# Kernel tuning notes

Hardware: AMD Instinct MI355X
Metric: run time of the kernel (lower is better)

Reference implementation:

```python
import jax, jax.numpy as jnp
import numpy as np

B, N, C, K = 16, 1024, 192, 9
H = 4 * C  # hidden of second MLP pair


def _gelu(x):
    return jax.nn.gelu(x, approximate=False)  # torch nn.GELU default is exact erf


def _mlp(x, w1, b1, w2, b2):
    # TwoLayerNN: Linear -> GELU -> Linear
    return _gelu(x @ w1.T + b1) @ w2.T + b2


def _linear_init(key, out_d, in_d):
    k1, k2 = jax.random.split(key)
    s = 1.0 / np.sqrt(in_d)
    w = jax.random.uniform(k1, (out_d, in_d), minval=-s, maxval=s, dtype=jnp.float32)
    b = jax.random.uniform(k2, (out_d,), minval=-s, maxval=s, dtype=jnp.float32)
    return w, b


def setup_inputs() -> dict:
    key = jax.random.key(0)
    ks = jax.random.split(key, 10)
    x = jax.random.normal(ks[0], (B, N, C), dtype=jnp.float32)
    il1_w1, il1_b1 = _linear_init(ks[1], C, C)
    il1_w2, il1_b2 = _linear_init(ks[2], C, C)
    ol1_w1, ol1_b1 = _linear_init(ks[3], C, C)
    ol1_w2, ol1_b2 = _linear_init(ks[4], C, C)
    il2_w1, il2_b1 = _linear_init(ks[5], H, C)
    il2_w2, il2_b2 = _linear_init(ks[6], C, H)
    ol2_w1, ol2_b1 = _linear_init(ks[7], H, C)
    ol2_w2, ol2_b2 = _linear_init(ks[8], C, H)
    fc_w, fc_b = _linear_init(ks[9], C, 2 * C)  # Conv1d(2C, C, 1) == Linear(2C->C)
    return dict(x=x,
                il1_w1=il1_w1, il1_b1=il1_b1, il1_w2=il1_w2, il1_b2=il1_b2,
                fc_w=fc_w, fc_b=fc_b,
                ol1_w1=ol1_w1, ol1_b1=ol1_b1, ol1_w2=ol1_w2, ol1_b2=ol1_b2,
                il2_w1=il2_w1, il2_b1=il2_b1, il2_w2=il2_w2, il2_b2=il2_b2,
                ol2_w1=ol2_w1, ol2_b1=ol2_b1, ol2_w2=ol2_w2, ol2_b2=ol2_b2)


def reference(x, il1_w1, il1_b1, il1_w2, il1_b2, fc_w, fc_b,
              ol1_w1, ol1_b1, ol1_w2, ol1_b2,
              il2_w1, il2_b1, il2_w2, il2_b2,
              ol2_w1, ol2_b1, ol2_w2, ol2_b2):
    Bx, Nx, Cx = x.shape
    # 1) dense similarity + KNN graph (indices only; no grad path through sim)
    sim = jnp.einsum('bnc,bmc->bnm', x, x)                       # [B,N,N]
    _, graph = jax.lax.top_k(sim, K)                             # [B,N,K] int32
    shortcut = x
    # 2) node transform then gather-max aggregation
    h = _mlp(x.reshape(Bx * Nx, Cx), il1_w1, il1_b1, il1_w2, il1_b2).reshape(Bx, Nx, Cx)
    nb = jnp.take_along_axis(h[:, None, :, :], graph[:, :, :, None], axis=2)  # [B,N,K,C]
    agg = jnp.max(nb - h[:, :, None, :], axis=2)                 # [B,N,C]
    # 3) stack along new last dim then flatten -> interleaved channels [x_c0,agg_c0,x_c1,...]
    cat = jnp.stack([h, agg], axis=-1).reshape(Bx, Nx, 2 * Cx)   # [B,N,2C]
    h = cat @ fc_w.T + fc_b                                      # Conv1d k=1 == Linear
    h = _mlp(_gelu(h).reshape(Bx * Nx, Cx), ol1_w1, ol1_b1, ol1_w2, ol1_b2).reshape(Bx, Nx, Cx)
    x1 = h + shortcut
    # 4) FFN block (two TwoLayerNNs with external GELU between them)
    f = _mlp(x1.reshape(Bx * Nx, Cx), il2_w1, il2_b1, il2_w2, il2_b2)
    f = _mlp(_gelu(f), ol2_w1, ol2_b1, ol2_w2, ol2_b2).reshape(Bx, Nx, Cx)
    return f + x1
```

## Files before the change

kernel.cpp:

```cpp
#include <hip/hip_runtime.h>
#include <hip/hip_bf16.h>
#include <math.h>

#define DEVINL __device__ __forceinline__

typedef __attribute__((ext_vector_type(4))) float f32x4;
typedef __attribute__((ext_vector_type(8))) short s16x8;

DEVINL unsigned short f2bf(float f) {
  union { float f; unsigned u; } v; v.f = f;
  unsigned r = v.u + 0x7FFFu + ((v.u >> 16) & 1u);
  return (unsigned short)(r >> 16);
}
DEVINL float bf2f(unsigned short s) {
  union { unsigned u; float f; } v; v.u = ((unsigned)s) << 16;
  return v.f;
}
DEVINL float gelu_exact(float x) {
  return 0.5f * x * (1.0f + erff(x * 0.70710678118654752f));
}

__global__ __launch_bounds__(256) void conv_kernel(const float* __restrict__ x,
                                                   unsigned short* __restrict__ xh,
                                                   unsigned short* __restrict__ xl) {
  int i = blockIdx.x * 256 + threadIdx.x;
  float4 v = ((const float4*)x)[i];
  float f[4] = {v.x, v.y, v.z, v.w};
  unsigned short h[4], l[4];
#pragma unroll
  for (int j = 0; j < 4; ++j) {
    h[j] = f2bf(f[j]);
    l[j] = f2bf(f[j] - bf2f(h[j]));
  }
  uint2 uh, ul;
  uh.x = (unsigned)h[0] | ((unsigned)h[1] << 16);
  uh.y = (unsigned)h[2] | ((unsigned)h[3] << 16);
  ul.x = (unsigned)l[0] | ((unsigned)l[1] << 16);
  ul.y = (unsigned)l[2] | ((unsigned)l[3] << 16);
  ((uint2*)xh)[i] = uh;
  ((uint2*)xl)[i] = ul;
}

__global__ __launch_bounds__(512)
#if __has_attribute(amdgpu_waves_per_eu)
__attribute__((amdgpu_waves_per_eu(4, 4)))
#endif
void simtopk_kernel(const unsigned short* __restrict__ xh,
                    const unsigned short* __restrict__ xl,
                    int* __restrict__ graph) {
  const int tid  = threadIdx.x;
  const int lane = tid & 63;
  const int w    = tid >> 6;
  const int rb   = blockIdx.x;
  const int b    = blockIdx.y;
  const int wm   = w >> 2, wn = w & 3;

  __shared__ __align__(16) char smem[57472];
  unsigned short* colsH = (unsigned short*)smem;
  unsigned short* colsL = (unsigned short*)(smem + 24576);
  float* simt = (float*)(smem + 49152);
  float* Lv = (float*)smem;
  int*   Li = (int*)(smem + 18432);
  float* Mv = (float*)(smem + 36864);
  int*   Mi = (int*)(smem + 41472);

  const unsigned short* xhb = xh + (size_t)b * (1024 * 192);
  const unsigned short* xlb = xl + (size_t)b * (1024 * 192);

  s16x8 ah[6], al[6];
#pragma unroll
  for (int ks = 0; ks < 6; ++ks) {
    int r = rb * 32 + wm * 16 + (lane & 15);
    size_t off = (size_t)r * 192 + ks * 32 + (lane >> 4) * 8;
    ah[ks] = *(const s16x8*)(xhb + off);
    al[ks] = *(const s16x8*)(xlb + off);
  }

  auto stage = [&](int ct) {
#pragma unroll
    for (int i = 0; i < 3; ++i) {
      int c = tid + i * 512;
      int row = c / 24, cc = c - row * 24;
      size_t goff = (size_t)(ct * 64 + row) * 192 + (size_t)((cc ^ (row & 7)) * 8);
      unsigned short* dstH = colsH + (size_t)c * 8;
      unsigned short* dstL = colsL + (size_t)c * 8;
      __builtin_amdgcn_global_load_lds((const __attribute__((address_space(1))) void*)(xhb + goff),
                                       (__attribute__((address_space(3))) void*)dstH, 16, 0, 0);
      __builtin_amdgcn_global_load_lds((const __attribute__((address_space(1))) void*)(xlb + goff),
                                       (__attribute__((address_space(3))) void*)dstL, 16, 0, 0);
    }
  };

  float tv[9]; int tix[9];
#pragma unroll
  for (int k = 0; k < 9; ++k) { tv[k] = -3.0e38f; tix[k] = 1 << 30; }

  stage(0);
  __syncthreads();

  for (int ct = 0; ct < 16; ++ct) {
    f32x4 a0 = 0, a1 = 0, a2 = 0;

#pragma unroll
    for (int ks = 0; ks < 6; ++ks) {
      const int chk = ks * 4 + (lane >> 4);
      const int rc  = wn * 16 + (lane & 15);
      const int si  = rc * 192 + ((chk ^ (rc & 7)) * 8);
      s16x8 bh = *(const s16x8*)&colsH[si];
      s16x8 bl = *(const s16x8*)&colsL[si];
      a0 = __builtin_amdgcn_mfma_f32_16x16x32_bf16(ah[ks], bh, a0, 0, 0, 0);
      a1 = __builtin_amdgcn_mfma_f32_16x16x32_bf16(ah[ks], bl, a1, 0, 0, 0);
      a2 = __builtin_amdgcn_mfma_f32_16x16x32_bf16(al[ks], bh, a2, 0, 0, 0);
    }

#pragma unroll
    for (int r = 0; r < 4; ++r) {
      int rr = wm * 16 + (lane >> 4) * 4 + r;
      int cc = wn * 16 + (lane & 15);
      simt[rr * 65 + cc] = a0[r] + a1[r] + a2[r];
    }
    __syncthreads();

    if (ct < 15) stage(ct + 1);

    {
      int r = tid >> 4, q = tid & 15;
#pragma unroll
      for (int j = 0; j < 4; ++j) {
        float v = simt[r * 65 + q * 4 + j];
        int   c = ct * 64 + q * 4 + j;
        if (v > tv[8]) {
          tv[8] = v; tix[8] = c;
#pragma unroll
          for (int s = 8; s > 0; --s) {
            if (tv[s] > tv[s - 1]) {
              float fv = tv[s]; tv[s] = tv[s - 1]; tv[s - 1] = fv;
              int   fi = tix[s]; tix[s] = tix[s - 1]; tix[s - 1] = fi;
            }
          }
        }
      }
    }
    __syncthreads();
  }

#pragma unroll
  for (int k = 0; k < 9; ++k) { Lv[tid * 9 + k] = tv[k]; Li[tid * 9 + k] = tix[k]; }
  __syncthreads();

  if (tid < 128) {
    int r = tid >> 2, p = tid & 3;
    float fv[9]; int fi[9];
#pragma unroll
    for (int k = 0; k < 9; ++k) { fv[k] = -3.0e38f; fi[k] = 1 << 30; }
    for (int s4 = 0; s4 < 4; ++s4) {
      int base = (r * 16 + p * 4 + s4) * 9;
#pragma unroll
      for (int k = 0; k < 9; ++k) {
        float v = Lv[base + k]; int c = Li[base + k];
        bool better = (v > fv[8]) || (v == fv[8] && c < fi[8]);
        if (better) {
          fv[8] = v; fi[8] = c;
#pragma unroll
          for (int s = 8; s > 0; --s) {
            bool up = (fv[s] > fv[s - 1]) || (fv[s] == fv[s - 1] && fi[s] < fi[s - 1]);
            if (up) {
              float a = fv[s]; fv[s] = fv[s - 1]; fv[s - 1] = a;
              int  ii = fi[s]; fi[s] = fi[s - 1]; fi[s - 1] = ii;
            }
          }
        }
      }
    }
#pragma unroll
    for (int k = 0; k < 9; ++k) { Mv[tid * 9 + k] = fv[k]; Mi[tid * 9 + k] = fi[k]; }
  }
  __syncthreads();

  if (tid < 32) {
    float fv[9]; int fi[9];
#pragma unroll
    for (int k = 0; k < 9; ++k) { fv[k] = -3.0e38f; fi[k] = 1 << 30; }
    for (int p = 0; p < 4; ++p) {
      int base = (tid * 4 + p) * 9;
#pragma unroll
      for (int k = 0; k < 9; ++k) {
        float v = Mv[base + k]; int c = Mi[base + k];
        bool better = (v > fv[8]) || (v == fv[8] && c < fi[8]);
        if (better) {
          fv[8] = v; fi[8] = c;
#pragma unroll
          for (int s = 8; s > 0; --s) {
            bool up = (fv[s] > fv[s - 1]) || (fv[s] == fv[s - 1] && fi[s] < fi[s - 1]);
            if (up) {
              float a = fv[s]; fv[s] = fv[s - 1]; fv[s - 1] = a;
              int  ii = fi[s]; fi[s] = fi[s - 1]; fi[s - 1] = ii;
            }
          }
        }
      }
    }
    int* gout = graph + ((size_t)b * 1024 + rb * 32 + tid) * 9;
#pragma unroll
    for (int k = 0; k < 9; ++k) gout[k] = fi[k];
  }
}

__global__ __launch_bounds__(256) void agg_kernel(const unsigned short* __restrict__ h,
                                                  const int* __restrict__ graph,
                                                  unsigned short* __restrict__ cat) {
  int gid  = blockIdx.x * 4 + (threadIdx.x >> 6);
  int lane = threadIdx.x & 63;
  int b = gid >> 10;
  int n = gid & 1023;
  const unsigned short* hb = h + (size_t)b * (1024 * 192);
  const int* g = graph + (size_t)gid * 9;
  float hn[3];
#pragma unroll
  for (int j = 0; j < 3; ++j) hn[j] = bf2f(hb[(size_t)n * 192 + lane + j * 64]);
  float ag[3] = {-3.0e38f, -3.0e38f, -3.0e38f};
  for (int k = 0; k < 9; ++k) {
    int idx = g[k];
#pragma unroll
    for (int j = 0; j < 3; ++j) {
      float v = bf2f(hb[(size_t)idx * 192 + lane + j * 64]) - hn[j];
      ag[j] = fmaxf(ag[j], v);
    }
  }
  unsigned* crow = (unsigned*)cat + (size_t)gid * 192;
#pragma unroll
  for (int j = 0; j < 3; ++j) {
    int c = lane + j * 64;
    crow[c] = (unsigned)f2bf(hn[j]) | ((unsigned)f2bf(ag[j]) << 16);
  }
}

template <bool GELU_, bool RESID>
__global__ __launch_bounds__(256) void gemm_kernel(const unsigned short* __restrict__ A,
                                                   const float* __restrict__ W,
                                                   const float* __restrict__ bias,
                                                   const float* __restrict__ resid,
                                                   unsigned short* __restrict__ outb,
                                                   float* __restrict__ outf,
                                                   int N, int K) {
  __shared__ unsigned short As[2][128 * 64];
  __shared__ unsigned short Ws[2][64 * 64];

  const int tid  = threadIdx.x;
  const int lane = tid & 63;
  const int w    = tid >> 6;
  const int m0   = blockIdx.x * 128;
  const int n0   = blockIdx.y * 64;

  auto stageA = [&](int buf, int kt) {
    const unsigned short* gA = A + (size_t)m0 * K + kt * 64;
#pragma unroll
    for (int i = 0; i < 4; ++i) {
      int chunk = w * 4 + i;
      const unsigned short* src = gA + (size_t)(chunk * 8 + (lane >> 3)) * K + (lane & 7) * 8;
      unsigned short* dst = &As[buf][chunk * 512];
      __builtin_amdgcn_global_load_lds((const __attribute__((address_space(1))) void*)src,
                                       (__attribute__((address_space(3))) void*)dst, 16, 0, 0);
    }
  };
  auto stageW = [&](int buf, int kt) {
#pragma unroll
    for (int i = 0; i < 4; ++i) {
      int idx = tid + i * 256;
      int n = idx >> 4, kq = idx & 15;
      float4 v = *(const float4*)(W + (size_t)(n0 + n) * K + kt * 64 + kq * 4);
      uint2 u;
      u.x = (unsigned)f2bf(v.x) | ((unsigned)f2bf(v.y) << 16);
      u.y = (unsigned)f2bf(v.z) | ((unsigned)f2bf(v.w) << 16);
      *(uint2*)&Ws[buf][n * 64 + kq * 4] = u;
    }
  };

  stageA(0, 0);
  stageW(0, 0);
  __syncthreads();

  const int wm = w >> 1, wn = w & 1;
  f32x4 acc[4][2];
#pragma unroll
  for (int a = 0; a < 4; ++a)
#pragma unroll
    for (int c = 0; c < 2; ++c) acc[a][c] = 0;

  const int nk = K >> 6;
  for (int kt = 0; kt < nk; ++kt) {
    const int cur = kt & 1;
    if (kt + 1 < nk) { stageA(cur ^ 1, kt + 1); stageW(cur ^ 1, kt + 1); }
#pragma unroll
    for (int ks = 0; ks < 2; ++ks) {
      const int ko = ks * 32 + (lane >> 4) * 8;
      s16x8 af[4], bfr[2];
#pragma unroll
      for (int m2 = 0; m2 < 4; ++m2)
        af[m2] = *(const s16x8*)&As[cur][(wm * 64 + m2 * 16 + (lane & 15)) * 64 + ko];
#pragma unroll
      for (int n2 = 0; n2 < 2; ++n2)
        bfr[n2] = *(const s16x8*)&Ws[cur][(wn * 32 + n2 * 16 + (lane & 15)) * 64 + ko];
#pragma unroll
      for (int m2 = 0; m2 < 4; ++m2)
#pragma unroll
        for (int n2 = 0; n2 < 2; ++n2)
          acc[m2][n2] = __builtin_amdgcn_mfma_f32_16x16x32_bf16(af[m2], bfr[n2], acc[m2][n2], 0, 0, 0);
    }
    __syncthreads();
  }

#pragma unroll
  for (int m2 = 0; m2 < 4; ++m2)
#pragma unroll
    for (int n2 = 0; n2 < 2; ++n2)
#pragma unroll
      for (int r = 0; r < 4; ++r) {
        int row = m0 + wm * 64 + m2 * 16 + (lane >> 4) * 4 + r;
        int col = n0 + wn * 32 + n2 * 16 + (lane & 15);
        float v = acc[m2][n2][r] + bias[col];
        if (GELU_) v = gelu_exact(v);
        if (RESID) v += resid[(size_t)row * N + col];
        size_t o = (size_t)row * N + col;
        if (outb) outb[o] = f2bf(v);
        if (outf) outf[o] = v;
      }
}

extern "C" void kernel_launch(void* const* d_in, const int* in_sizes, int n_in,
                              void* d_out, int out_size, void* d_ws, size_t ws_size,
                              hipStream_t stream) {
  (void)in_sizes; (void)n_in; (void)out_size; (void)ws_size;
  const float* x      = (const float*)d_in[0];
  const float* il1_w1 = (const float*)d_in[1];
  const float* il1_b1 = (const float*)d_in[2];
  const float* il1_w2 = (const float*)d_in[3];
  const float* il1_b2 = (const float*)d_in[4];
  const float* fc_w   = (const float*)d_in[5];
  const float* fc_b   = (const float*)d_in[6];
  const float* ol1_w1 = (const float*)d_in[7];
  const float* ol1_b1 = (const float*)d_in[8];
  const float* ol1_w2 = (const float*)d_in[9];
  const float* ol1_b2 = (const float*)d_in[10];
  const float* il2_w1 = (const float*)d_in[11];
  const float* il2_b1 = (const float*)d_in[12];
  const float* il2_w2 = (const float*)d_in[13];
  const float* il2_b2 = (const float*)d_in[14];
  const float* ol2_w1 = (const float*)d_in[15];
  const float* ol2_b1 = (const float*)d_in[16];
  const float* ol2_w2 = (const float*)d_in[17];
  const float* ol2_b2 = (const float*)d_in[18];

  char* ws = (char*)d_ws;
  const size_t SZ = 16384ull * 192 * 2;
  unsigned short* xbf  = (unsigned short*)(ws);
  unsigned short* t13  = (unsigned short*)(ws + SZ);
  unsigned short* hbuf = (unsigned short*)(ws + 2 * SZ);
  unsigned short* t2   = (unsigned short*)(ws + 3 * SZ);
  unsigned short* x1b  = (unsigned short*)(ws + 4 * SZ);
  unsigned short* catg = (unsigned short*)(ws + 5 * SZ);
  float*          x1f  = (float*)(ws + 7 * SZ);
  unsigned short* uv   = (unsigned short*)(ws + 9 * SZ);
  unsigned short* xlo  = uv;
  int*            graph = (int*)(ws + 13 * SZ);

  conv_kernel<<<3072, 256, 0, stream>>>(x, xbf, xlo);
  simtopk_kernel<<<dim3(32, 16), 512, 0, stream>>>(xbf, xlo, graph);
  gemm_kernel<true,  false><<<dim3(128, 3), 256, 0, stream>>>(xbf, il1_w1, il1_b1, nullptr, t13, nullptr, 192, 192);
  gemm_kernel<false, false><<<dim3(128, 3), 256, 0, stream>>>(t13, il1_w2, il1_b2, nullptr, hbuf, nullptr, 192, 192);
  agg_kernel<<<4096, 256, 0, stream>>>(hbuf, graph, catg);
  gemm_kernel<true,  false><<<dim3(128, 3), 256, 0, stream>>>(catg, fc_w, fc_b, nullptr, t2, nullptr, 192, 384);
  gemm_kernel<true,  false><<<dim3(128, 3), 256, 0, stream>>>(t2, ol1_w1, ol1_b1, nullptr, t13, nullptr, 192, 192);
  gemm_kernel<false, true ><<<dim3(128, 3), 256, 0, stream>>>(t13, ol1_w2, ol1_b2, x, x1b, x1f, 192, 192);
  gemm_kernel<true,  false><<<dim3(128, 12), 256, 0, stream>>>(x1b, il2_w1, il2_b1, nullptr, uv, nullptr, 768, 192);
  gemm_kernel<true,  false><<<dim3(128, 3), 256, 0, stream>>>(uv, il2_w2, il2_b2, nullptr, catg, nullptr, 192, 768);
  gemm_kernel<true,  false><<<dim3(128, 12), 256, 0, stream>>>(catg, ol2_w1, ol2_b1, nullptr, uv, nullptr, 768, 192);
  gemm_kernel<false, true ><<<dim3(128, 3), 256, 0, stream>>>(uv, ol2_w2, ol2_b2, x1f, nullptr, (float*)d_out, 192, 768);
}
```

Before: 266.4 us.

## Preconvert weights to bf16, swizzle GEMM LDS, and top-k directly from accumulators

New measurement: 241.6 us. 9.3% less time.

```diff
diff --git a/kernel.cpp b/kernel.cpp
--- a/kernel.cpp
+++ b/kernel.cpp
@@ -39,6 +39,23 @@
   ul.y = (unsigned)l[2] | ((unsigned)l[3] << 16);
   ((uint2*)xh)[i] = uh;
   ((uint2*)xl)[i] = ul;
+}
+
+struct WArgs {
+  const float* s[9];
+  unsigned short* d[9];
+  int n4[9];
+};
+__global__ __launch_bounds__(256) void wconv_kernel(WArgs a) {
+  int seg = blockIdx.y;
+  int i = blockIdx.x * 256 + threadIdx.x;
+  if (i >= a.n4[seg]) return;
+  float4 v = ((const float4*)a.s[seg])[i];
+  float f[4] = {v.x, v.y, v.z, v.w};
+  uint2 u;
+  u.x = (unsigned)f2bf(f[0]) | ((unsigned)f2bf(f[1]) << 16);
+  u.y = (unsigned)f2bf(f[2]) | ((unsigned)f2bf(f[3]) << 16);
+  ((uint2*)a.d[seg])[i] = u;
 }
 
 __global__ __launch_bounds__(512)
@@ -51,14 +68,16 @@
   const int tid  = threadIdx.x;
   const int lane = tid & 63;
   const int w    = tid >> 6;
-  const int rb   = blockIdx.x;
-  const int b    = blockIdx.y;
   const int wm   = w >> 2, wn = w & 3;
 
-  __shared__ __align__(16) char smem[57472];
+  const int lin  = blockIdx.y * 32 + blockIdx.x;
+  const int work = (lin & 7) * 64 + (lin >> 3);
+  const int rb   = work & 31;
+  const int b    = work >> 5;
+
+  __shared__ __align__(16) char smem[49152];
   unsigned short* colsH = (unsigned short*)smem;
   unsigned short* colsL = (unsigned short*)(smem + 24576);
-  float* simt = (float*)(smem + 49152);
   float* Lv = (float*)smem;
   int*   Li = (int*)(smem + 18432);
   float* Mv = (float*)(smem + 36864);
@@ -108,27 +127,20 @@
       const int si  = rc * 192 + ((chk ^ (rc & 7)) * 8);
       s16x8 bh = *(const s16x8*)&colsH[si];
       s16x8 bl = *(const s16x8*)&colsL[si];
-      a0 = __builtin_amdgcn_mfma_f32_16x16x32_bf16(ah[ks], bh, a0, 0, 0, 0);
-      a1 = __builtin_amdgcn_mfma_f32_16x16x32_bf16(ah[ks], bl, a1, 0, 0, 0);
-      a2 = __builtin_amdgcn_mfma_f32_16x16x32_bf16(al[ks], bh, a2, 0, 0, 0);
-    }
-
-#pragma unroll
-    for (int r = 0; r < 4; ++r) {
-      int rr = wm * 16 + (lane >> 4) * 4 + r;
-      int cc = wn * 16 + (lane & 15);
-      simt[rr * 65 + cc] = a0[r] + a1[r] + a2[r];
+      a0 = __builtin_amdgcn_mfma_f32_16x16x32_bf16(bh, ah[ks], a0, 0, 0, 0);
+      a1 = __builtin_amdgcn_mfma_f32_16x16x32_bf16(bl, ah[ks], a1, 0, 0, 0);
+      a2 = __builtin_amdgcn_mfma_f32_16x16x32_bf16(bh, al[ks], a2, 0, 0, 0);
     }
     __syncthreads();
 
     if (ct < 15) stage(ct + 1);
 
     {
-      int r = tid >> 4, q = tid & 15;
-#pragma unroll
-      for (int j = 0; j < 4; ++j) {
-        float v = simt[r * 65 + q * 4 + j];
-        int   c = ct * 64 + q * 4 + j;
+      int cbase = ct * 64 + wn * 16 + (lane >> 4) * 4;
+#pragma unroll
+      for (int r = 0; r < 4; ++r) {
+        float v = a0[r] + a1[r] + a2[r];
+        int   c = cbase + r;
         if (v > tv[8]) {
           tv[8] = v; tix[8] = c;
 #pragma unroll
@@ -144,8 +156,13 @@
     __syncthreads();
   }
 
-#pragma unroll
-  for (int k = 0; k < 9; ++k) { Lv[tid * 9 + k] = tv[k]; Li[tid * 9 + k] = tix[k]; }
+  {
+    int rowloc  = wm * 16 + (lane & 15);
+    int listid  = wn * 4 + (lane >> 4);
+    int lbase   = (rowloc * 16 + listid) * 9;
+#pragma unroll
+    for (int k = 0; k < 9; ++k) { Lv[lbase + k] = tv[k]; Li[lbase + k] = tix[k]; }
+  }
   __syncthreads();
 
   if (tid < 128) {
@@ -237,7 +254,7 @@
 
 template <bool GELU_, bool RESID>
 __global__ __launch_bounds__(256) void gemm_kernel(const unsigned short* __restrict__ A,
-                                                   const float* __restrict__ W,
+                                                   const unsigned short* __restrict__ W,
                                                    const float* __restrict__ bias,
                                                    const float* __restrict__ resid,
                                                    unsigned short* __restrict__ outb,
@@ -253,11 +270,12 @@
   const int n0   = blockIdx.y * 64;
 
   auto stageA = [&](int buf, int kt) {
-    const unsigned short* gA = A + (size_t)m0 * K + kt * 64;
 #pragma unroll
     for (int i = 0; i < 4; ++i) {
       int chunk = w * 4 + i;
-      const unsigned short* src = gA + (size_t)(chunk * 8 + (lane >> 3)) * K + (lane & 7) * 8;
+      int row = chunk * 8 + (lane >> 3);
+      const unsigned short* src = A + (size_t)(m0 + row) * K + kt * 64
+                                    + (((lane & 7) ^ (row & 7)) * 8);
       unsigned short* dst = &As[buf][chunk * 512];
       __builtin_amdgcn_global_load_lds((const __attribute__((address_space(1))) void*)src,
                                        (__attribute__((address_space(3))) void*)dst, 16, 0, 0);
@@ -265,14 +283,14 @@
   };
   auto stageW = [&](int buf, int kt) {
 #pragma unroll
-    for (int i = 0; i < 4; ++i) {
-      int idx = tid + i * 256;
-      int n = idx >> 4, kq = idx & 15;
-      float4 v = *(const float4*)(W + (size_t)(n0 + n) * K + kt * 64 + kq * 4);
-      uint2 u;
-      u.x = (unsigned)f2bf(v.x) | ((unsigned)f2bf(v.y) << 16);
-      u.y = (unsigned)f2bf(v.z) | ((unsigned)f2bf(v.w) << 16);
-      *(uint2*)&Ws[buf][n * 64 + kq * 4] = u;
+    for (int i = 0; i < 2; ++i) {
+      int chunk = w * 2 + i;
+      int row = chunk * 8 + (lane >> 3);
+      const unsigned short* src = W + (size_t)(n0 + row) * K + kt * 64
+                                    + (((lane & 7) ^ (row & 7)) * 8);
+      unsigned short* dst = &Ws[buf][chunk * 512];
+      __builtin_amdgcn_global_load_lds((const __attribute__((address_space(1))) void*)src,
+                                       (__attribute__((address_space(3))) void*)dst, 16, 0, 0);
     }
   };
 
@@ -293,14 +311,18 @@
     if (kt + 1 < nk) { stageA(cur ^ 1, kt + 1); stageW(cur ^ 1, kt + 1); }
 #pragma unroll
     for (int ks = 0; ks < 2; ++ks) {
-      const int ko = ks * 32 + (lane >> 4) * 8;
+      const int kc = ks * 4 + (lane >> 4);
       s16x8 af[4], bfr[2];
 #pragma unroll
-      for (int m2 = 0; m2 < 4; ++m2)
-        af[m2] = *(const s16x8*)&As[cur][(wm * 64 + m2 * 16 + (lane & 15)) * 64 + ko];
-#pragma unroll
-      for (int n2 = 0; n2 < 2; ++n2)
-        bfr[n2] = *(const s16x8*)&Ws[cur][(wn * 32 + n2 * 16 + (lane & 15)) * 64 + ko];
+      for (int m2 = 0; m2 < 4; ++m2) {
+        int row = wm * 64 + m2 * 16 + (lane & 15);
+        af[m2] = *(const s16x8*)&As[cur][row * 64 + ((kc ^ (row & 7)) * 8)];
+      }
+#pragma unroll
+      for (int n2 = 0; n2 < 2; ++n2) {
+        int rw = wn * 32 + n2 * 16 + (lane & 15);
+        bfr[n2] = *(const s16x8*)&Ws[cur][rw * 64 + ((kc ^ (rw & 7)) * 8)];
+      }
 #pragma unroll
       for (int m2 = 0; m2 < 4; ++m2)
 #pragma unroll
@@ -363,17 +385,40 @@
   unsigned short* uv   = (unsigned short*)(ws + 9 * SZ);
   unsigned short* xlo  = uv;
   int*            graph = (int*)(ws + 13 * SZ);
+  unsigned short* wb   = (unsigned short*)(ws + 13 * SZ + (1 << 20));
+
+  unsigned short* il1_w1b = wb;
+  unsigned short* il1_w2b = wb + 36864;
+  unsigned short* fcb     = wb + 73728;
+  unsigned short* ol1_w1b = wb + 147456;
+  unsigned short* ol1_w2b = wb + 184320;
+  unsigned short* il2_w1b = wb + 221184;
+  unsigned short* il2_w2b = wb + 368640;
+  unsigned short* ol2_w1b = wb + 516096;
+  unsigned short* ol2_w2b = wb + 663552;
+
+  WArgs wa;
+  wa.s[0] = il1_w1; wa.d[0] = il1_w1b; wa.n4[0] = 36864 / 4;
+  wa.s[1] = il1_w2; wa.d[1] = il1_w2b; wa.n4[1] = 36864 / 4;
+  wa.s[2] = fc_w;   wa.d[2] = fcb;     wa.n4[2] = 73728 / 4;
+  wa.s[3] = ol1_w1; wa.d[3] = ol1_w1b; wa.n4[3] = 36864 / 4;
+  wa.s[4] = ol1_w2; wa.d[4] = ol1_w2b; wa.n4[4] = 36864 / 4;
+  wa.s[5] = il2_w1; wa.d[5] = il2_w1b; wa.n4[5] = 147456 / 4;
+  wa.s[6] = il2_w2; wa.d[6] = il2_w2b; wa.n4[6] = 147456 / 4;
+  wa.s[7] = ol2_w1; wa.d[7] = ol2_w1b; wa.n4[7] = 147456 / 4;
+  wa.s[8] = ol2_w2; wa.d[8] = ol2_w2b; wa.n4[8] = 147456 / 4;
 
   conv_kernel<<<3072, 256, 0, stream>>>(x, xbf, xlo);
+  wconv_kernel<<<dim3(144, 9), 256, 0, stream>>>(wa);
   simtopk_kernel<<<dim3(32, 16), 512, 0, stream>>>(xbf, xlo, graph);
-  gemm_kernel<true,  false><<<dim3(128, 3), 256, 0, stream>>>(xbf, il1_w1, il1_b1, nullptr, t13, nullptr, 192, 192);
-  gemm_kernel<false, false><<<dim3(128, 3), 256, 0, stream>>>(t13, il1_w2, il1_b2, nullptr, hbuf, nullptr, 192, 192);
+  gemm_kernel<true,  false><<<dim3(128, 3), 256, 0, stream>>>(xbf, il1_w1b, il1_b1, nullptr, t13, nullptr, 192, 192);
+  gemm_kernel<false, false><<<dim3(128, 3), 256, 0, stream>>>(t13, il1_w2b, il1_b2, nullptr, hbuf, nullptr, 192, 192);
   agg_kernel<<<4096, 256, 0, stream>>>(hbuf, graph, catg);
-  gemm_kernel<true,  false><<<dim3(128, 3), 256, 0, stream>>>(catg, fc_w, fc_b, nullptr, t2, nullptr, 192, 384);
-  gemm_kernel<true,  false><<<dim3(128, 3), 256, 0, stream>>>(t2, ol1_w1, ol1_b1, nullptr, t13, nullptr, 192, 192);
-  gemm_kernel<false, true ><<<dim3(128, 3), 256, 0, stream>>>(t13, ol1_w2, ol1_b2, x, x1b, x1f, 192, 192);
-  gemm_kernel<true,  false><<<dim3(128, 12), 256, 0, stream>>>(x1b, il2_w1, il2_b1, nullptr, uv, nullptr, 768, 192);
-  gemm_kernel<true,  false><<<dim3(128, 3), 256, 0, stream>>>(uv, il2_w2, il2_b2, nullptr, catg, nullptr, 192, 768);
-  gemm_kernel<true,  false><<<dim3(128, 12), 256, 0, stream>>>(catg, ol2_w1, ol2_b1, nullptr, uv, nullptr, 768, 192);
-  gemm_kernel<false, true ><<<dim3(128, 3), 256, 0, stream>>>(uv, ol2_w2, ol2_b2, x1f, nullptr, (float*)d_out, 192, 768);
-}
+  gemm_kernel<true,  false><<<dim3(128, 3), 256, 0, stream>>>(catg, fcb, fc_b, nullptr, t2, nullptr, 192, 384);
+  gemm_kernel<true,  false><<<dim3(128, 3), 256, 0, stream>>>(t2, ol1_w1b, ol1_b1, nullptr, t13, nullptr, 192, 192);
+  gemm_kernel<false, true ><<<dim3(128, 3), 256, 0, stream>>>(t13, ol1_w2b, ol1_b2, x, x1b, x1f, 192, 192);
+  gemm_kernel<true,  false><<<dim3(128, 12), 256, 0, stream>>>(x1b, il2_w1b, il2_b1, nullptr, uv, nullptr, 768, 192);
+  gemm_kernel<true,  false><<<dim3(128, 3), 256, 0, stream>>>(uv, il2_w2b, il2_b2, nullptr, catg, nullptr, 192, 768);
+  gemm_kernel<true,  false><<<dim3(128, 12), 256, 0, stream>>>(catg, ol2_w1b, ol2_b1, nullptr, uv, nullptr, 768, 192);
+  gemm_kernel<false, true ><<<dim3(128, 3), 256, 0, stream>>>(uv, ol2_w2b, ol2_b2, x1f, nullptr, (float*)d_out, 192, 768);
+}
```
